# Kernel optimization log

Measured on AMD Instinct MI355X. Metric: run time of the kernel, lower is better.

The kernel has to match this reference:

```python
import jax, jax.numpy as jnp
import numpy as np

N, D_IN, D_OUT, E = 50000, 64, 64, 800000
NEG_SLOPE = 0.2  # PyG GATConv default leaky-relu slope


def setup_inputs() -> dict:
    key = jax.random.key(0)
    ks = jax.random.split(key, 11)
    s_in = 1.0 / np.sqrt(D_IN)
    s_out = 1.0 / np.sqrt(D_OUT)
    return {
        "x": jax.random.normal(ks[0], (N, D_IN), jnp.float32),
        "edge_index": jax.random.randint(ks[1], (2, E), 0, N, jnp.int32),
        "h": jax.random.normal(ks[2], (N, D_OUT), jnp.float32) * 0.1,
        "c": jax.random.normal(ks[3], (N, D_OUT), jnp.float32) * 0.1,
        "W": jax.random.normal(ks[4], (4, D_IN, D_OUT), jnp.float32) * s_in,
        "b": jax.random.normal(ks[5], (4, 1, D_OUT), jnp.float32) * 0.01,
        "Wsrc": jax.random.normal(ks[6], (4, D_OUT, D_OUT), jnp.float32) * s_out,
        "Wdst": jax.random.normal(ks[7], (4, D_OUT, D_OUT), jnp.float32) * s_out,
        "att_src": jax.random.normal(ks[8], (4, D_OUT), jnp.float32) * 0.1,
        "att_dst": jax.random.normal(ks[9], (4, D_OUT), jnp.float32) * 0.1,
        "gat_b": jax.random.normal(ks[10], (4, D_OUT), jnp.float32) * 0.01,
    }


def _gat(h, src, dst, Ws, Wd, a_s, a_d, bg, n):
    """GATConv(heads=1, add_self_loops=False) on edges src->dst."""
    hs = h @ Ws                      # [N, D] source-side projection
    hd = h @ Wd                      # [N, D] dest-side projection
    alpha_s = hs @ a_s               # [N]
    alpha_d = hd @ a_d               # [N]
    e = jax.nn.leaky_relu(alpha_s[src] + alpha_d[dst], NEG_SLOPE)  # [E]
    # numerically stable segment softmax over incoming edges per dst node
    m = jax.ops.segment_max(e, dst, num_segments=n)
    ex = jnp.exp(e - m[dst])
    denom = jax.ops.segment_sum(ex, dst, num_segments=n)
    w = ex / denom[dst]              # [E] attention weights
    out = jax.ops.segment_sum(w[:, None] * hs[src], dst, num_segments=n)
    return out + bg


def reference(x, edge_index, h, c, W, b, Wsrc, Wdst, att_src, att_dst, gat_b):
    src, dst = edge_index[0], edge_index[1]
    n = x.shape[0]

    def gate(g, act):
        pre = x @ W[g] + _gat(h, src, dst, Wsrc[g], Wdst[g],
                              att_src[g], att_dst[g], gat_b[g], n) + b[g]
        return act(pre)

    i = gate(0, jax.nn.sigmoid)
    f = gate(1, jax.nn.sigmoid)
    t = gate(2, jnp.tanh)
    c_new = f * c + i * t
    o = gate(3, jax.nn.sigmoid)   # output gate conv uses the OLD hidden state h
    h_new = o * jnp.tanh(c_new)
    return (h_new, c_new)
```

## Files before the change

kernel.cpp:

```cpp
#include <hip/hip_runtime.h>
#include <math.h>

#define NEG_SLOPE 0.2f

typedef float  f32x4 __attribute__((ext_vector_type(4)));
typedef short  s16x8 __attribute__((ext_vector_type(8)));

__device__ __forceinline__ unsigned short bfr(float a){
  unsigned u = __float_as_uint(a);
  return (unsigned short)((u + 0x7FFFu + ((u>>16)&1u)) >> 16);
}
__device__ __forceinline__ float bf2f(unsigned short s){
  return __uint_as_float(((unsigned)s)<<16);
}
__device__ __forceinline__ ushort4 packf4(float4 v){
  ushort4 r; r.x=bfr(v.x); r.y=bfr(v.y); r.z=bfr(v.z); r.w=bfr(v.w); return r;
}

__global__ void k_wvec_pack(const float* __restrict__ Wsrc, const float* __restrict__ Wdst,
                            const float* __restrict__ Wmain,
                            const float* __restrict__ att_src, const float* __restrict__ att_dst,
                            float* __restrict__ wvec,
                            unsigned short* __restrict__ pw, unsigned short* __restrict__ ps){
  int tid = threadIdx.x;
  if (blockIdx.x == 0){
    int v = tid >> 6, t = tid & 63;
    const float* M = (v<4) ? (Wsrc + v*4096) : (Wdst + (v-4)*4096);
    const float* a = (v<4) ? (att_src + v*64) : (att_dst + (v-4)*64);
    float s = 0.f;
    for (int k=0;k<64;++k) s += M[t*64+k]*a[k];
    wvec[v*64+t] = s;
  } else {
    int vv = (blockIdx.x-1)*512 + tid;
    if (vv < 2048){
      int l = vv & 63, u = vv >> 6;
      int ct = u & 3, ks = (u>>2)&1, g = u>>3;
      int col = ct*16 + (l&15);
      int r0  = ks*32 + (l>>4)*8;
      #pragma unroll
      for (int j=0;j<8;++j){
        pw[vv*8+j] = bfr(Wmain[g*4096 + (r0+j)*64 + col]);
        ps[vv*8+j] = bfr(Wsrc [g*4096 + (r0+j)*64 + col]);
      }
    }
  }
}

__global__ __launch_bounds__(256) void k_pack(
    const float* __restrict__ x, const float* __restrict__ h,
    const float* __restrict__ wvec,
    unsigned short* __restrict__ xb, unsigned short* __restrict__ hb,
    float* __restrict__ alphas, int N){
  __shared__ float hl[32*65];
  __shared__ float wl[8*65];
  int tid = threadIdx.x;
  int nbase = blockIdx.x*32;
  int nlim = min(32, N-nbase);
  int cnt = nlim*16;
  {
    const float4* hsrc = (const float4*)(h + (size_t)nbase*64);
    const float4* xsrc = (const float4*)(x + (size_t)nbase*64);
    ushort4* hdst = (ushort4*)(hb + (size_t)nbase*64);
    ushort4* xdst = (ushort4*)(xb + (size_t)nbase*64);
    for (int i=tid; i<cnt; i+=256){
      float4 v = hsrc[i];
      int n = i>>4, t4 = (i&15)*4;
      float* d = hl + n*65 + t4;
      d[0]=v.x; d[1]=v.y; d[2]=v.z; d[3]=v.w;
      hdst[i] = packf4(v);
      xdst[i] = packf4(xsrc[i]);
    }
    for (int i=tid; i<512; i+=256) wl[(i>>6)*65 + (i&63)] = wvec[i];
  }
  __syncthreads();
  int v = tid & 7, n = tid >> 3;
  if (n < nlim){
    const float* hp = hl + n*65;
    const float* wp = wl + v*65;
    float s = 0.f;
    #pragma unroll
    for (int t=0;t<64;++t) s += hp[t]*wp[t];
    alphas[(size_t)(nbase+n)*8 + v] = s;
  }
}

__global__ __launch_bounds__(256) void k_bcount(
    const int* __restrict__ ei, int* __restrict__ bcnt, int shift, int E){
  __shared__ int c[128];
  int tid = threadIdx.x;
  for (int i=tid;i<128;i+=256) c[i]=0;
  __syncthreads();
  int Q = E >> 2;
  const int4* d4 = (const int4*)(ei + E);
  long gs = (long)gridDim.x*256;
  for (long q=(long)blockIdx.x*256+tid; q<Q; q+=gs){
    int4 d = d4[q];
    atomicAdd(&c[d.x>>shift],1); atomicAdd(&c[d.y>>shift],1);
    atomicAdd(&c[d.z>>shift],1); atomicAdd(&c[d.w>>shift],1);
  }
  int tail = E - (Q<<2);
  if (blockIdx.x==0 && tid<tail) atomicAdd(&c[ei[E+(Q<<2)+tid]>>shift],1);
  __syncthreads();
  for (int i=tid;i<128;i+=256) if (c[i]) atomicAdd(&bcnt[i], c[i]);
}

__global__ void k_bscan(const int* __restrict__ bcnt, int* __restrict__ bbase,
                        int* __restrict__ bfill, int* __restrict__ rowptr,
                        int nbuck, int N, int E){
  __shared__ int s[128];
  int tid = threadIdx.x;
  int x = (tid<nbuck) ? bcnt[tid] : 0;
  s[tid] = x;
  __syncthreads();
  for (int off=1; off<128; off<<=1){
    int t = (tid>=off) ? s[tid-off] : 0;
    __syncthreads();
    s[tid] += t;
    __syncthreads();
  }
  if (tid<nbuck){ int e = s[tid]-x; bbase[tid]=e; bfill[tid]=e; }
  if (tid==0){ bbase[nbuck]=E; rowptr[N]=E; }
}

__global__ __launch_bounds__(256) void k_bin(
    const int* __restrict__ ei, int* __restrict__ bfill,
    int2* __restrict__ binned, int shift, int E){
  __shared__ int2 buf[2048];
  __shared__ int cnt[128], off[128], gbase[128];
  int tid = threadIdx.x;
  int c0 = blockIdx.x*2048;
  int m = min(2048, E - c0);
  if (m <= 0) return;
  for (int i=tid; i<128; i+=256) cnt[i] = 0;
  __syncthreads();
  int myb[8], myslot[8], mysrc[8], mydst[8];
  #pragma unroll
  for (int j=0;j<8;++j){
    int k = tid + j*256;
    if (k < m){
      int e = c0 + k;
      mysrc[j] = ei[e];
      mydst[j] = ei[E+e];
      int bkt = mydst[j] >> shift;
      myb[j] = bkt;
      myslot[j] = atomicAdd(&cnt[bkt], 1);
    } else myb[j] = -1;
  }
  __syncthreads();
  if (tid == 0){
    int acc = 0;
    for (int i=0;i<128;++i){ off[i] = acc; acc += cnt[i]; }
  }
  __syncthreads();
  #pragma unroll
  for (int j=0;j<8;++j)
    if (myb[j] >= 0) buf[off[myb[j]] + myslot[j]] = make_int2(mysrc[j], mydst[j]);
  if (tid < 128 && cnt[tid] > 0) gbase[tid] = atomicAdd(&bfill[tid], cnt[tid]);
  __syncthreads();
  for (int i=tid; i<m; i+=256){
    int2 p = buf[i];
    int bkt = p.y >> shift;
    binned[gbase[bkt] + (i - off[bkt])] = p;
  }
}

__global__ __launch_bounds__(1024) void k_place(
    const int2* __restrict__ binned, const int* __restrict__ bbase,
    int* __restrict__ rowptr, int* __restrict__ csr_src, int shift, int N){
  __shared__ int cnt[1024];
  __shared__ int tsum[1024];
  int tid = threadIdx.x;
  int d0 = blockIdx.x << shift;
  if (d0 >= N) return;
  int dpb = 1 << shift;
  int dlim = min(dpb, N - d0);
  if (tid < dpb) cnt[tid] = 0;
  __syncthreads();
  int base = bbase[blockIdx.x], end = bbase[blockIdx.x+1];
  for (int i = base + tid; i < end; i += 1024)
    atomicAdd(&cnt[binned[i].y - d0], 1);
  __syncthreads();
  int xv = (tid < dpb) ? cnt[tid] : 0;
  tsum[tid] = xv;
  __syncthreads();
  for (int off=1; off<1024; off<<=1){
    int t = (tid>=off) ? tsum[tid-off] : 0;
    __syncthreads();
    tsum[tid] += t;
    __syncthreads();
  }
  if (tid < dpb) cnt[tid] = tsum[tid] - xv + base;
  __syncthreads();
  if (tid < dlim) rowptr[d0+tid] = cnt[tid];
  __syncthreads();
  for (int i = base + tid; i < end; i += 1024){
    int2 p = binned[i];
    int pos = atomicAdd(&cnt[p.y - d0], 1);
    csr_src[pos] = p.x;
  }
}

__global__ __launch_bounds__(256) void k_agg(
    const int* __restrict__ csr_src, const int* __restrict__ rowptr,
    const float* __restrict__ alphas,
    const unsigned short* __restrict__ hb, unsigned short* __restrict__ aggb, int N){
  __shared__ float4 wb4[4][64];
  __shared__ int    sb[4][64];
  int wave = threadIdx.x>>6, lane = threadIdx.x&63;
  int dst = blockIdx.x*4 + wave;
  if (dst >= N) return;
  int base = rowptr[dst];
  int d = rowptr[dst+1] - base;
  float4 ad = ((const float4*)alphas)[dst*2+1];
  float ss0=0.f,ss1=0.f,ss2=0.f,ss3=0.f;
  float a0=0.f,a1=0.f,a2=0.f,a3=0.f;
  for (int c0=0; c0<d; c0+=64){
    int cnt = min(64, d-c0);
    if (lane < cnt){
      int s = csr_src[base+c0+lane];
      float4 as = ((const float4*)alphas)[(size_t)s*2];
      float e0=as.x+ad.x; e0 = e0>0.f ? e0 : NEG_SLOPE*e0; float x0=__expf(e0); ss0+=x0;
      float e1=as.y+ad.y; e1 = e1>0.f ? e1 : NEG_SLOPE*e1; float x1=__expf(e1); ss1+=x1;
      float e2=as.z+ad.z; e2 = e2>0.f ? e2 : NEG_SLOPE*e2; float x2=__expf(e2); ss2+=x2;
      float e3=as.w+ad.w; e3 = e3>0.f ? e3 : NEG_SLOPE*e3; float x3=__expf(e3); ss3+=x3;
      sb[wave][lane] = s;
      wb4[wave][lane] = make_float4(x0,x1,x2,x3);
    }
    asm volatile("" ::: "memory");
    int j = 0;
    for (; j+3 < cnt; j += 4){
      int s0_ = sb[wave][j],   s1_ = sb[wave][j+1];
      int s2_ = sb[wave][j+2], s3_ = sb[wave][j+3];
      float4 w0_ = wb4[wave][j],   w1_ = wb4[wave][j+1];
      float4 w2_ = wb4[wave][j+2], w3_ = wb4[wave][j+3];
      float h0_ = bf2f(hb[(size_t)s0_*64 + lane]);
      float h1_ = bf2f(hb[(size_t)s1_*64 + lane]);
      float h2_ = bf2f(hb[(size_t)s2_*64 + lane]);
      float h3_ = bf2f(hb[(size_t)s3_*64 + lane]);
      a0 += w0_.x*h0_; a1 += w0_.y*h0_; a2 += w0_.z*h0_; a3 += w0_.w*h0_;
      a0 += w1_.x*h1_; a1 += w1_.y*h1_; a2 += w1_.z*h1_; a3 += w1_.w*h1_;
      a0 += w2_.x*h2_; a1 += w2_.y*h2_; a2 += w2_.z*h2_; a3 += w2_.w*h2_;
      a0 += w3_.x*h3_; a1 += w3_.y*h3_; a2 += w3_.z*h3_; a3 += w3_.w*h3_;
    }
    for (; j < cnt; ++j){
      int s = sb[wave][j];
      float4 w = wb4[wave][j];
      float hv = bf2f(hb[(size_t)s*64 + lane]);
      a0 += w.x*hv; a1 += w.y*hv; a2 += w.z*hv; a3 += w.w*hv;
    }
    asm volatile("" ::: "memory");
  }
  #pragma unroll
  for (int off=32; off; off>>=1){
    ss0 += __shfl_xor(ss0, off, 64);
    ss1 += __shfl_xor(ss1, off, 64);
    ss2 += __shfl_xor(ss2, off, 64);
    ss3 += __shfl_xor(ss3, off, 64);
  }
  size_t o = (size_t)dst*64 + lane;
  size_t NE = (size_t)N*64;
  if (d>0){
    aggb[o]      = bfr(a0/ss0);
    aggb[NE+o]   = bfr(a1/ss1);
    aggb[2*NE+o] = bfr(a2/ss2);
    aggb[3*NE+o] = bfr(a3/ss3);
  } else {
    aggb[o] = 0; aggb[NE+o] = 0; aggb[2*NE+o] = 0; aggb[3*NE+o] = 0;
  }
}

__global__ __launch_bounds__(256) void k_fused(
    const unsigned short* __restrict__ xb, const unsigned short* __restrict__ aggb,
    const unsigned short* __restrict__ pw, const unsigned short* __restrict__ ps,
    const float* __restrict__ b, const float* __restrict__ gat_b,
    const float* __restrict__ c, float* __restrict__ out, int N){
  __shared__ float Pl[4][32][68];
  int tid = threadIdx.x, g = tid>>6, l = tid&63;
  int lr = l & 15;
  int lq = l >> 4;
  int nbase = blockIdx.x*32;
  int nlim = min(32, N-nbase);

  s16x8 BW[2][4], BS[2][4];
  #pragma unroll
  for (int ks=0; ks<2; ++ks){
    #pragma unroll
    for (int ct=0; ct<4; ++ct){
      size_t idx = ((size_t)((g*2+ks)*4+ct)*64 + l)*8;
      BW[ks][ct] = *(const s16x8*)(pw + idx);
      BS[ks][ct] = *(const s16x8*)(ps + idx);
    }
  }

  s16x8 AX[2][2], AG[2][2];
  #pragma unroll
  for (int rt=0; rt<2; ++rt){
    int row = nbase + rt*16 + lr;
    if (row >= N) row = N-1;
    #pragma unroll
    for (int ks=0; ks<2; ++ks){
      AX[rt][ks] = *(const s16x8*)(xb   + (size_t)row*64 + ks*32 + lq*8);
      AG[rt][ks] = *(const s16x8*)(aggb + ((size_t)g*N + row)*64 + ks*32 + lq*8);
    }
  }

  #pragma unroll
  for (int rt=0; rt<2; ++rt){
    #pragma unroll
    for (int ct=0; ct<4; ++ct){
      int col = ct*16 + lr;
      float bias = b[g*64 + col] + gat_b[g*64 + col];
      f32x4 acc = {bias, bias, bias, bias};
      #pragma unroll
      for (int ks=0; ks<2; ++ks){
        acc = __builtin_amdgcn_mfma_f32_16x16x32_bf16(AX[rt][ks], BW[ks][ct], acc, 0,0,0);
        acc = __builtin_amdgcn_mfma_f32_16x16x32_bf16(AG[rt][ks], BS[ks][ct], acc, 0,0,0);
      }
      #pragma unroll
      for (int r=0;r<4;++r)
        Pl[g][rt*16 + lq*4 + r][col] = acc[r];
    }
  }
  __syncthreads();

  size_t NE = (size_t)N*64;
  #pragma unroll
  for (int n=0; n<8; ++n){
    int node = g*8 + n;
    if (node < nlim){
      size_t o = (size_t)(nbase + node)*64 + l;
      float p0 = Pl[0][node][l];
      float p1 = Pl[1][node][l];
      float p2 = Pl[2][node][l];
      float p3 = Pl[3][node][l];
      float ig = 1.f/(1.f + __expf(-p0));
      float fg = 1.f/(1.f + __expf(-p1));
      float tg = tanhf(p2);
      float og = 1.f/(1.f + __expf(-p3));
      float cn = fg*c[o] + ig*tg;
      out[o]      = og*tanhf(cn);
      out[NE + o] = cn;
    }
  }
}

extern "C" void kernel_launch(void* const* d_in, const int* in_sizes, int n_in,
                              void* d_out, int out_size, void* d_ws, size_t ws_size,
                              hipStream_t stream){
  const float* x       = (const float*)d_in[0];
  const int*   ei      = (const int*)d_in[1];
  const float* h       = (const float*)d_in[2];
  const float* c       = (const float*)d_in[3];
  const float* W       = (const float*)d_in[4];
  const float* b       = (const float*)d_in[5];
  const float* Wsrc    = (const float*)d_in[6];
  const float* Wdst    = (const float*)d_in[7];
  const float* att_src = (const float*)d_in[8];
  const float* att_dst = (const float*)d_in[9];
  const float* gat_b   = (const float*)d_in[10];
  float* out = (float*)d_out;

  int N = in_sizes[0] / 64;
  int E = in_sizes[1] / 2;

  int shift = 9;
  while (((N + (1<<shift) - 1) >> shift) > 128) shift++;
  int nbuck = (N + (1<<shift) - 1) >> shift;

  unsigned short* aggb = (unsigned short*)d_ws;
  unsigned short* xb   = aggb + (size_t)4*N*64;
  unsigned short* hb   = xb   + (size_t)N*64;
  unsigned short* pw   = hb   + (size_t)N*64;
  unsigned short* ps   = pw   + 16384;
  float* alphas = (float*)(ps + 16384);
  int* csr_src  = (int*)(alphas + (size_t)N*8);
  int2* binned  = (int2*)(csr_src + ((E+3)&~3));
  int* rowptr   = (int*)(binned + E);
  int* bcnt     = rowptr + N + 1;
  int* bbase    = bcnt + 128;
  int* bfill    = bbase + 129;
  float* wvec   = (float*)(bfill + 128);

  hipMemsetAsync(bcnt, 0, 128*sizeof(int), stream);
  k_wvec_pack<<<9, 512, 0, stream>>>(Wsrc, Wdst, W, att_src, att_dst, wvec, pw, ps);
  k_pack  <<<(N+31)/32, 256, 0, stream>>>(x, h, wvec, xb, hb, alphas, N);
  k_bcount<<<256, 256, 0, stream>>>(ei, bcnt, shift, E);
  k_bscan <<<1, 128, 0, stream>>>(bcnt, bbase, bfill, rowptr, nbuck, N, E);
  k_bin   <<<(E + 2047)/2048, 256, 0, stream>>>(ei, bfill, binned, shift, E);
  k_place <<<nbuck, 1024, 0, stream>>>(binned, bbase, rowptr, csr_src, shift, N);
  k_agg   <<<(N+3)/4, 256, 0, stream>>>(csr_src, rowptr, alphas, hb, aggb, N);
  k_fused <<<(N+31)/32, 256, 0, stream>>>(xb, aggb, pw, ps, b, gat_b, c, out, N);
}
```

Before: 127.4 us.

## Fuse bucket counting into pack kernel and process two destinations per wave

The memset is replaced by zeroing the bucket counters inside k_wvec_pack, and the separate k_bcount kernel is merged into k_pack, which now also histograms the destination indices. This removes two launches from the chain. k_agg now has each wave handle two destination nodes at once, which raises memory-level parallelism on the gathers but does extra work when the two degrees differ. Each wave also uses more registers.

```diff
diff --git a/kernel.cpp b/kernel.cpp
--- a/kernel.cpp
+++ b/kernel.cpp
@@ -20,10 +20,11 @@
 __global__ void k_wvec_pack(const float* __restrict__ Wsrc, const float* __restrict__ Wdst,
                             const float* __restrict__ Wmain,
                             const float* __restrict__ att_src, const float* __restrict__ att_dst,
-                            float* __restrict__ wvec,
+                            float* __restrict__ wvec, int* __restrict__ bcnt,
                             unsigned short* __restrict__ pw, unsigned short* __restrict__ ps){
   int tid = threadIdx.x;
   if (blockIdx.x == 0){
+    if (tid < 128) bcnt[tid] = 0;
     int v = tid >> 6, t = tid & 63;
     const float* M = (v<4) ? (Wsrc + v*4096) : (Wdst + (v-4)*4096);
     const float* a = (v<4) ? (att_src + v*64) : (att_dst + (v-4)*64);
@@ -48,15 +49,17 @@
 
 __global__ __launch_bounds__(256) void k_pack(
     const float* __restrict__ x, const float* __restrict__ h,
-    const float* __restrict__ wvec,
+    const float* __restrict__ wvec, const int* __restrict__ ei,
     unsigned short* __restrict__ xb, unsigned short* __restrict__ hb,
-    float* __restrict__ alphas, int N){
+    float* __restrict__ alphas, int* __restrict__ bcnt, int shift, int N, int E){
   __shared__ float hl[32*65];
   __shared__ float wl[8*65];
+  __shared__ int   cb[128];
   int tid = threadIdx.x;
   int nbase = blockIdx.x*32;
   int nlim = min(32, N-nbase);
   int cnt = nlim*16;
+  if (tid < 128) cb[tid] = 0;
   {
     const float4* hsrc = (const float4*)(h + (size_t)nbase*64);
     const float4* xsrc = (const float4*)(x + (size_t)nbase*64);
@@ -82,26 +85,18 @@
     for (int t=0;t<64;++t) s += hp[t]*wp[t];
     alphas[(size_t)(nbase+n)*8 + v] = s;
   }
-}
-
-__global__ __launch_bounds__(256) void k_bcount(
-    const int* __restrict__ ei, int* __restrict__ bcnt, int shift, int E){
-  __shared__ int c[128];
-  int tid = threadIdx.x;
-  for (int i=tid;i<128;i+=256) c[i]=0;
-  __syncthreads();
   int Q = E >> 2;
   const int4* d4 = (const int4*)(ei + E);
   long gs = (long)gridDim.x*256;
   for (long q=(long)blockIdx.x*256+tid; q<Q; q+=gs){
     int4 d = d4[q];
-    atomicAdd(&c[d.x>>shift],1); atomicAdd(&c[d.y>>shift],1);
-    atomicAdd(&c[d.z>>shift],1); atomicAdd(&c[d.w>>shift],1);
+    atomicAdd(&cb[d.x>>shift],1); atomicAdd(&cb[d.y>>shift],1);
+    atomicAdd(&cb[d.z>>shift],1); atomicAdd(&cb[d.w>>shift],1);
   }
   int tail = E - (Q<<2);
-  if (blockIdx.x==0 && tid<tail) atomicAdd(&c[ei[E+(Q<<2)+tid]>>shift],1);
-  __syncthreads();
-  for (int i=tid;i<128;i+=256) if (c[i]) atomicAdd(&bcnt[i], c[i]);
+  if (blockIdx.x == 0 && tid < tail) atomicAdd(&cb[ei[E+(Q<<2)+tid]>>shift],1);
+  __syncthreads();
+  if (tid < 128 && cb[tid]) atomicAdd(&bcnt[tid], cb[tid]);
 }
 
 __global__ void k_bscan(const int* __restrict__ bcnt, int* __restrict__ bbase,
@@ -204,68 +199,109 @@
     const int* __restrict__ csr_src, const int* __restrict__ rowptr,
     const float* __restrict__ alphas,
     const unsigned short* __restrict__ hb, unsigned short* __restrict__ aggb, int N){
-  __shared__ float4 wb4[4][64];
-  __shared__ int    sb[4][64];
+  __shared__ float4 wb4[4][2][64];
+  __shared__ int    sb[4][2][64];
   int wave = threadIdx.x>>6, lane = threadIdx.x&63;
-  int dst = blockIdx.x*4 + wave;
-  if (dst >= N) return;
-  int base = rowptr[dst];
-  int d = rowptr[dst+1] - base;
-  float4 ad = ((const float4*)alphas)[dst*2+1];
-  float ss0=0.f,ss1=0.f,ss2=0.f,ss3=0.f;
-  float a0=0.f,a1=0.f,a2=0.f,a3=0.f;
-  for (int c0=0; c0<d; c0+=64){
-    int cnt = min(64, d-c0);
-    if (lane < cnt){
-      int s = csr_src[base+c0+lane];
-      float4 as = ((const float4*)alphas)[(size_t)s*2];
-      float e0=as.x+ad.x; e0 = e0>0.f ? e0 : NEG_SLOPE*e0; float x0=__expf(e0); ss0+=x0;
-      float e1=as.y+ad.y; e1 = e1>0.f ? e1 : NEG_SLOPE*e1; float x1=__expf(e1); ss1+=x1;
-      float e2=as.z+ad.z; e2 = e2>0.f ? e2 : NEG_SLOPE*e2; float x2=__expf(e2); ss2+=x2;
-      float e3=as.w+ad.w; e3 = e3>0.f ? e3 : NEG_SLOPE*e3; float x3=__expf(e3); ss3+=x3;
-      sb[wave][lane] = s;
-      wb4[wave][lane] = make_float4(x0,x1,x2,x3);
+  int dst0 = blockIdx.x*8 + wave*2;
+  if (dst0 >= N) return;
+  int dst1 = dst0 + 1;
+  bool has1 = dst1 < N;
+  int base0 = rowptr[dst0];
+  int d0 = rowptr[dst0+1] - base0;
+  int base1 = has1 ? rowptr[dst1] : 0;
+  int d1 = has1 ? rowptr[dst1+1] - base1 : 0;
+  float4 ad0 = ((const float4*)alphas)[(size_t)dst0*2+1];
+  float4 ad1 = has1 ? ((const float4*)alphas)[(size_t)dst1*2+1] : make_float4(0,0,0,0);
+  float p00=0.f,p01=0.f,p02=0.f,p03=0.f, q00=0.f,q01=0.f,q02=0.f,q03=0.f;
+  float a00=0.f,a01=0.f,a02=0.f,a03=0.f, b00=0.f,b01=0.f,b02=0.f,b03=0.f;
+  int dmax = max(d0, d1);
+  for (int c0=0; c0<dmax; c0+=64){
+    {
+      int rem = d0 - c0;
+      int s = 0; float4 w = make_float4(0,0,0,0);
+      if (lane < rem){
+        s = csr_src[base0+c0+lane];
+        float4 as = ((const float4*)alphas)[(size_t)s*2];
+        float e0=as.x+ad0.x; e0 = e0>0.f ? e0 : NEG_SLOPE*e0; w.x=__expf(e0);
+        float e1=as.y+ad0.y; e1 = e1>0.f ? e1 : NEG_SLOPE*e1; w.y=__expf(e1);
+        float e2=as.z+ad0.z; e2 = e2>0.f ? e2 : NEG_SLOPE*e2; w.z=__expf(e2);
+        float e3=as.w+ad0.w; e3 = e3>0.f ? e3 : NEG_SLOPE*e3; w.w=__expf(e3);
+      }
+      p00+=w.x; p01+=w.y; p02+=w.z; p03+=w.w;
+      sb[wave][0][lane] = s;
+      wb4[wave][0][lane] = w;
+    }
+    {
+      int rem = d1 - c0;
+      int s = 0; float4 w = make_float4(0,0,0,0);
+      if (lane < rem){
+        s = csr_src[base1+c0+lane];
+        float4 as = ((const float4*)alphas)[(size_t)s*2];
+        float e0=as.x+ad1.x; e0 = e0>0.f ? e0 : NEG_SLOPE*e0; w.x=__expf(e0);
+        float e1=as.y+ad1.y; e1 = e1>0.f ? e1 : NEG_SLOPE*e1; w.y=__expf(e1);
+        float e2=as.z+ad1.z; e2 = e2>0.f ? e2 : NEG_SLOPE*e2; w.z=__expf(e2);
+        float e3=as.w+ad1.w; e3 = e3>0.f ? e3 : NEG_SLOPE*e3; w.w=__expf(e3);
+      }
+      q00+=w.x; q01+=w.y; q02+=w.z; q03+=w.w;
+      sb[wave][1][lane] = s;
+      wb4[wave][1][lane] = w;
     }
     asm volatile("" ::: "memory");
+    int cc = min(64, dmax - c0);
     int j = 0;
-    for (; j+3 < cnt; j += 4){
-      int s0_ = sb[wave][j],   s1_ = sb[wave][j+1];
-      int s2_ = sb[wave][j+2], s3_ = sb[wave][j+3];
-      float4 w0_ = wb4[wave][j],   w1_ = wb4[wave][j+1];
-      float4 w2_ = wb4[wave][j+2], w3_ = wb4[wave][j+3];
-      float h0_ = bf2f(hb[(size_t)s0_*64 + lane]);
-      float h1_ = bf2f(hb[(size_t)s1_*64 + lane]);
-      float h2_ = bf2f(hb[(size_t)s2_*64 + lane]);
-      float h3_ = bf2f(hb[(size_t)s3_*64 + lane]);
-      a0 += w0_.x*h0_; a1 += w0_.y*h0_; a2 += w0_.z*h0_; a3 += w0_.w*h0_;
-      a0 += w1_.x*h1_; a1 += w1_.y*h1_; a2 += w1_.z*h1_; a3 += w1_.w*h1_;
-      a0 += w2_.x*h2_; a1 += w2_.y*h2_; a2 += w2_.z*h2_; a3 += w2_.w*h2_;
-      a0 += w3_.x*h3_; a1 += w3_.y*h3_; a2 += w3_.z*h3_; a3 += w3_.w*h3_;
-    }
-    for (; j < cnt; ++j){
-      int s = sb[wave][j];
-      float4 w = wb4[wave][j];
-      float hv = bf2f(hb[(size_t)s*64 + lane]);
-      a0 += w.x*hv; a1 += w.y*hv; a2 += w.z*hv; a3 += w.w*hv;
+    for (; j+1 < cc; j += 2){
+      int   sa0 = sb[wave][0][j],  sa1 = sb[wave][0][j+1];
+      int   sc0 = sb[wave][1][j],  sc1 = sb[wave][1][j+1];
+      float4 wa0 = wb4[wave][0][j], wa1 = wb4[wave][0][j+1];
+      float4 wc0 = wb4[wave][1][j], wc1 = wb4[wave][1][j+1];
+      float ha0 = bf2f(hb[(size_t)sa0*64 + lane]);
+      float ha1 = bf2f(hb[(size_t)sa1*64 + lane]);
+      float hc0 = bf2f(hb[(size_t)sc0*64 + lane]);
+      float hc1 = bf2f(hb[(size_t)sc1*64 + lane]);
+      a00 += wa0.x*ha0; a01 += wa0.y*ha0; a02 += wa0.z*ha0; a03 += wa0.w*ha0;
+      a00 += wa1.x*ha1; a01 += wa1.y*ha1; a02 += wa1.z*ha1; a03 += wa1.w*ha1;
+      b00 += wc0.x*hc0; b01 += wc0.y*hc0; b02 += wc0.z*hc0; b03 += wc0.w*hc0;
+      b00 += wc1.x*hc1; b01 += wc1.y*hc1; b02 += wc1.z*hc1; b03 += wc1.w*hc1;
+    }
+    for (; j < cc; ++j){
+      int   sa = sb[wave][0][j],  sc = sb[wave][1][j];
+      float4 wa = wb4[wave][0][j], wc = wb4[wave][1][j];
+      float ha = bf2f(hb[(size_t)sa*64 + lane]);
+      float hc = bf2f(hb[(size_t)sc*64 + lane]);
+      a00 += wa.x*ha; a01 += wa.y*ha; a02 += wa.z*ha; a03 += wa.w*ha;
+      b00 += wc.x*hc; b01 += wc.y*hc; b02 += wc.z*hc; b03 += wc.w*hc;
     }
     asm volatile("" ::: "memory");
   }
   #pragma unroll
   for (int off=32; off; off>>=1){
-    ss0 += __shfl_xor(ss0, off, 64);
-    ss1 += __shfl_xor(ss1, off, 64);
-    ss2 += __shfl_xor(ss2, off, 64);
-    ss3 += __shfl_xor(ss3, off, 64);
-  }
-  size_t o = (size_t)dst*64 + lane;
+    p00 += __shfl_xor(p00, off, 64); p01 += __shfl_xor(p01, off, 64);
+    p02 += __shfl_xor(p02, off, 64); p03 += __shfl_xor(p03, off, 64);
+    q00 += __shfl_xor(q00, off, 64); q01 += __shfl_xor(q01, off, 64);
+    q02 += __shfl_xor(q02, off, 64); q03 += __shfl_xor(q03, off, 64);
+  }
   size_t NE = (size_t)N*64;
-  if (d>0){
-    aggb[o]      = bfr(a0/ss0);
-    aggb[NE+o]   = bfr(a1/ss1);
-    aggb[2*NE+o] = bfr(a2/ss2);
-    aggb[3*NE+o] = bfr(a3/ss3);
-  } else {
-    aggb[o] = 0; aggb[NE+o] = 0; aggb[2*NE+o] = 0; aggb[3*NE+o] = 0;
+  {
+    size_t o = (size_t)dst0*64 + lane;
+    if (d0>0){
+      aggb[o]      = bfr(a00/p00);
+      aggb[NE+o]   = bfr(a01/p01);
+      aggb[2*NE+o] = bfr(a02/p02);
+      aggb[3*NE+o] = bfr(a03/p03);
+    } else {
+      aggb[o]=0; aggb[NE+o]=0; aggb[2*NE+o]=0; aggb[3*NE+o]=0;
+    }
+  }
+  if (has1){
+    size_t o = (size_t)dst1*64 + lane;
+    if (d1>0){
+      aggb[o]      = bfr(b00/q00);
+      aggb[NE+o]   = bfr(b01/q01);
+      aggb[2*NE+o] = bfr(b02/q02);
+      aggb[3*NE+o] = bfr(b03/q03);
+    } else {
+      aggb[o]=0; aggb[NE+o]=0; aggb[2*NE+o]=0; aggb[3*NE+o]=0;
+    }
   }
 }
 
@@ -381,13 +417,11 @@
   int* bfill    = bbase + 129;
   float* wvec   = (float*)(bfill + 128);
 
-  hipMemsetAsync(bcnt, 0, 128*sizeof(int), stream);
-  k_wvec_pack<<<9, 512, 0, stream>>>(Wsrc, Wdst, W, att_src, att_dst, wvec, pw, ps);
-  k_pack  <<<(N+31)/32, 256, 0, stream>>>(x, h, wvec, xb, hb, alphas, N);
-  k_bcount<<<256, 256, 0, stream>>>(ei, bcnt, shift, E);
+  k_wvec_pack<<<9, 512, 0, stream>>>(Wsrc, Wdst, W, att_src, att_dst, wvec, bcnt, pw, ps);
+  k_pack  <<<(N+31)/32, 256, 0, stream>>>(x, h, wvec, ei, xb, hb, alphas, bcnt, shift, N, E);
   k_bscan <<<1, 128, 0, stream>>>(bcnt, bbase, bfill, rowptr, nbuck, N, E);
   k_bin   <<<(E + 2047)/2048, 256, 0, stream>>>(ei, bfill, binned, shift, E);
   k_place <<<nbuck, 1024, 0, stream>>>(binned, bbase, rowptr, csr_src, shift, N);
-  k_agg   <<<(N+3)/4, 256, 0, stream>>>(csr_src, rowptr, alphas, hb, aggb, N);
+  k_agg   <<<(N+7)/8, 256, 0, stream>>>(csr_src, rowptr, alphas, hb, aggb, N);
   k_fused <<<(N+31)/32, 256, 0, stream>>>(xb, aggb, pw, ps, b, gat_b, c, out, N);
 }
```

Measured after the change: 133.9 us. 5.2% more time.

## Precompute edge attention weights in placement kernel and fuse bucket count into pack

Applied to the files above, without the earlier changes.

Edge attention exponentials are now computed in the CSR placement kernel, which already visits every edge, and stored as fp16 per-edge weights. The aggregation kernel no longer does the random gather of source alphas or the exp math. The bucket-count kernel is folded into the pack kernel, and the memset is replaced by zeroing inside the weight-pack kernel, which cuts two launches. The trade-off is an extra E×8-byte weight write and read, plus fp16 rounding of the unnormalized exp weights, which could overflow if logits are large.

```diff
diff --git a/kernel.cpp b/kernel.cpp
--- a/kernel.cpp
+++ b/kernel.cpp
@@ -5,6 +5,8 @@
 
 typedef float  f32x4 __attribute__((ext_vector_type(4)));
 typedef short  s16x8 __attribute__((ext_vector_type(8)));
+
+union H4 { ushort4 u; _Float16 h[4]; };
 
 __device__ __forceinline__ unsigned short bfr(float a){
   unsigned u = __float_as_uint(a);
@@ -20,10 +22,11 @@
 __global__ void k_wvec_pack(const float* __restrict__ Wsrc, const float* __restrict__ Wdst,
                             const float* __restrict__ Wmain,
                             const float* __restrict__ att_src, const float* __restrict__ att_dst,
-                            float* __restrict__ wvec,
+                            float* __restrict__ wvec, int* __restrict__ bcnt,
                             unsigned short* __restrict__ pw, unsigned short* __restrict__ ps){
   int tid = threadIdx.x;
   if (blockIdx.x == 0){
+    if (tid < 128) bcnt[tid] = 0;
     int v = tid >> 6, t = tid & 63;
     const float* M = (v<4) ? (Wsrc + v*4096) : (Wdst + (v-4)*4096);
     const float* a = (v<4) ? (att_src + v*64) : (att_dst + (v-4)*64);
@@ -48,15 +51,17 @@
 
 __global__ __launch_bounds__(256) void k_pack(
     const float* __restrict__ x, const float* __restrict__ h,
-    const float* __restrict__ wvec,
+    const float* __restrict__ wvec, const int* __restrict__ ei,
     unsigned short* __restrict__ xb, unsigned short* __restrict__ hb,
-    float* __restrict__ alphas, int N){
+    float* __restrict__ alphas, int* __restrict__ bcnt, int shift, int N, int E){
   __shared__ float hl[32*65];
   __shared__ float wl[8*65];
+  __shared__ int   cb[128];
   int tid = threadIdx.x;
   int nbase = blockIdx.x*32;
   int nlim = min(32, N-nbase);
   int cnt = nlim*16;
+  if (tid < 128) cb[tid] = 0;
   {
     const float4* hsrc = (const float4*)(h + (size_t)nbase*64);
     const float4* xsrc = (const float4*)(x + (size_t)nbase*64);
@@ -82,26 +87,18 @@
     for (int t=0;t<64;++t) s += hp[t]*wp[t];
     alphas[(size_t)(nbase+n)*8 + v] = s;
   }
-}
-
-__global__ __launch_bounds__(256) void k_bcount(
-    const int* __restrict__ ei, int* __restrict__ bcnt, int shift, int E){
-  __shared__ int c[128];
-  int tid = threadIdx.x;
-  for (int i=tid;i<128;i+=256) c[i]=0;
-  __syncthreads();
   int Q = E >> 2;
   const int4* d4 = (const int4*)(ei + E);
   long gs = (long)gridDim.x*256;
   for (long q=(long)blockIdx.x*256+tid; q<Q; q+=gs){
     int4 d = d4[q];
-    atomicAdd(&c[d.x>>shift],1); atomicAdd(&c[d.y>>shift],1);
-    atomicAdd(&c[d.z>>shift],1); atomicAdd(&c[d.w>>shift],1);
+    atomicAdd(&cb[d.x>>shift],1); atomicAdd(&cb[d.y>>shift],1);
+    atomicAdd(&cb[d.z>>shift],1); atomicAdd(&cb[d.w>>shift],1);
   }
   int tail = E - (Q<<2);
-  if (blockIdx.x==0 && tid<tail) atomicAdd(&c[ei[E+(Q<<2)+tid]>>shift],1);
-  __syncthreads();
-  for (int i=tid;i<128;i+=256) if (c[i]) atomicAdd(&bcnt[i], c[i]);
+  if (blockIdx.x == 0 && tid < tail) atomicAdd(&cb[ei[E+(Q<<2)+tid]>>shift],1);
+  __syncthreads();
+  if (tid < 128 && cb[tid]) atomicAdd(&bcnt[tid], cb[tid]);
 }
 
 __global__ void k_bscan(const int* __restrict__ bcnt, int* __restrict__ bbase,
@@ -166,15 +163,19 @@
 
 __global__ __launch_bounds__(1024) void k_place(
     const int2* __restrict__ binned, const int* __restrict__ bbase,
-    int* __restrict__ rowptr, int* __restrict__ csr_src, int shift, int N){
+    const float* __restrict__ alphas,
+    int* __restrict__ rowptr, int* __restrict__ csr_src,
+    ushort4* __restrict__ csr_w, int shift, int N){
   __shared__ int cnt[1024];
   __shared__ int tsum[1024];
+  __shared__ float4 adl[1024];
   int tid = threadIdx.x;
   int d0 = blockIdx.x << shift;
   if (d0 >= N) return;
   int dpb = 1 << shift;
   int dlim = min(dpb, N - d0);
   if (tid < dpb) cnt[tid] = 0;
+  if (tid < dlim) adl[tid] = ((const float4*)alphas)[(size_t)(d0+tid)*2 + 1];
   __syncthreads();
   int base = bbase[blockIdx.x], end = bbase[blockIdx.x+1];
   for (int i = base + tid; i < end; i += 1024)
@@ -195,14 +196,27 @@
   __syncthreads();
   for (int i = base + tid; i < end; i += 1024){
     int2 p = binned[i];
-    int pos = atomicAdd(&cnt[p.y - d0], 1);
+    int loc = p.y - d0;
+    int pos = atomicAdd(&cnt[loc], 1);
+    float4 as = ((const float4*)alphas)[(size_t)p.x*2];
+    float4 ad = adl[loc];
+    float e0=as.x+ad.x; e0 = e0>0.f ? e0 : NEG_SLOPE*e0;
+    float e1=as.y+ad.y; e1 = e1>0.f ? e1 : NEG_SLOPE*e1;
+    float e2=as.z+ad.z; e2 = e2>0.f ? e2 : NEG_SLOPE*e2;
+    float e3=as.w+ad.w; e3 = e3>0.f ? e3 : NEG_SLOPE*e3;
+    H4 t;
+    t.h[0] = (_Float16)__expf(e0);
+    t.h[1] = (_Float16)__expf(e1);
+    t.h[2] = (_Float16)__expf(e2);
+    t.h[3] = (_Float16)__expf(e3);
     csr_src[pos] = p.x;
+    csr_w[pos] = t.u;
   }
 }
 
 __global__ __launch_bounds__(256) void k_agg(
-    const int* __restrict__ csr_src, const int* __restrict__ rowptr,
-    const float* __restrict__ alphas,
+    const int* __restrict__ csr_src, const ushort4* __restrict__ csr_w,
+    const int* __restrict__ rowptr,
     const unsigned short* __restrict__ hb, unsigned short* __restrict__ aggb, int N){
   __shared__ float4 wb4[4][64];
   __shared__ int    sb[4][64];
@@ -211,21 +225,19 @@
   if (dst >= N) return;
   int base = rowptr[dst];
   int d = rowptr[dst+1] - base;
-  float4 ad = ((const float4*)alphas)[dst*2+1];
   float ss0=0.f,ss1=0.f,ss2=0.f,ss3=0.f;
   float a0=0.f,a1=0.f,a2=0.f,a3=0.f;
   for (int c0=0; c0<d; c0+=64){
     int cnt = min(64, d-c0);
+    int s = 0; float4 w = make_float4(0,0,0,0);
     if (lane < cnt){
-      int s = csr_src[base+c0+lane];
-      float4 as = ((const float4*)alphas)[(size_t)s*2];
-      float e0=as.x+ad.x; e0 = e0>0.f ? e0 : NEG_SLOPE*e0; float x0=__expf(e0); ss0+=x0;
-      float e1=as.y+ad.y; e1 = e1>0.f ? e1 : NEG_SLOPE*e1; float x1=__expf(e1); ss1+=x1;
-      float e2=as.z+ad.z; e2 = e2>0.f ? e2 : NEG_SLOPE*e2; float x2=__expf(e2); ss2+=x2;
-      float e3=as.w+ad.w; e3 = e3>0.f ? e3 : NEG_SLOPE*e3; float x3=__expf(e3); ss3+=x3;
-      sb[wave][lane] = s;
-      wb4[wave][lane] = make_float4(x0,x1,x2,x3);
-    }
+      s = csr_src[base+c0+lane];
+      H4 t; t.u = csr_w[base+c0+lane];
+      w = make_float4((float)t.h[0], (float)t.h[1], (float)t.h[2], (float)t.h[3]);
+    }
+    ss0 += w.x; ss1 += w.y; ss2 += w.z; ss3 += w.w;
+    sb[wave][lane] = s;
+    wb4[wave][lane] = w;
     asm volatile("" ::: "memory");
     int j = 0;
     for (; j+3 < cnt; j += 4){
@@ -243,10 +255,10 @@
       a0 += w3_.x*h3_; a1 += w3_.y*h3_; a2 += w3_.z*h3_; a3 += w3_.w*h3_;
     }
     for (; j < cnt; ++j){
-      int s = sb[wave][j];
-      float4 w = wb4[wave][j];
-      float hv = bf2f(hb[(size_t)s*64 + lane]);
-      a0 += w.x*hv; a1 += w.y*hv; a2 += w.z*hv; a3 += w.w*hv;
+      int sj = sb[wave][j];
+      float4 wj = wb4[wave][j];
+      float hv = bf2f(hb[(size_t)sj*64 + lane]);
+      a0 += wj.x*hv; a1 += wj.y*hv; a2 += wj.z*hv; a3 += wj.w*hv;
     }
     asm volatile("" ::: "memory");
   }
@@ -375,19 +387,18 @@
   float* alphas = (float*)(ps + 16384);
   int* csr_src  = (int*)(alphas + (size_t)N*8);
   int2* binned  = (int2*)(csr_src + ((E+3)&~3));
-  int* rowptr   = (int*)(binned + E);
+  ushort4* csr_w= (ushort4*)(binned + E);
+  int* rowptr   = (int*)(csr_w + E);
   int* bcnt     = rowptr + N + 1;
   int* bbase    = bcnt + 128;
   int* bfill    = bbase + 129;
   float* wvec   = (float*)(bfill + 128);
 
-  hipMemsetAsync(bcnt, 0, 128*sizeof(int), stream);
-  k_wvec_pack<<<9, 512, 0, stream>>>(Wsrc, Wdst, W, att_src, att_dst, wvec, pw, ps);
-  k_pack  <<<(N+31)/32, 256, 0, stream>>>(x, h, wvec, xb, hb, alphas, N);
-  k_bcount<<<256, 256, 0, stream>>>(ei, bcnt, shift, E);
+  k_wvec_pack<<<9, 512, 0, stream>>>(Wsrc, Wdst, W, att_src, att_dst, wvec, bcnt, pw, ps);
+  k_pack  <<<(N+31)/32, 256, 0, stream>>>(x, h, wvec, ei, xb, hb, alphas, bcnt, shift, N, E);
   k_bscan <<<1, 128, 0, stream>>>(bcnt, bbase, bfill, rowptr, nbuck, N, E);
   k_bin   <<<(E + 2047)/2048, 256, 0, stream>>>(ei, bfill, binned, shift, E);
-  k_place <<<nbuck, 1024, 0, stream>>>(binned, bbase, rowptr, csr_src, shift, N);
-  k_agg   <<<(N+3)/4, 256, 0, stream>>>(csr_src, rowptr, alphas, hb, aggb, N);
+  k_place <<<nbuck, 1024, 0, stream>>>(binned, bbase, alphas, rowptr, csr_src, csr_w, shift, N);
+  k_agg   <<<(N+3)/4, 256, 0, stream>>>(csr_src, csr_w, rowptr, hb, aggb, N);
   k_fused <<<(N+31)/32, 256, 0, stream>>>(xb, aggb, pw, ps, b, gat_b, c, out, N);
 }
```

After: 144.4 us. 1.13x slower.

## Fuse bucket counting into pack kernel, drop memset, unroll aggregation by eight

Applied to the files above, without the earlier changes.

The destination-bucket histogram is folded into k_pack, so each of its many blocks counts a grid-strided slice of edges into shared memory before flushing to global. The bcnt zeroing moves into k_wvec_pack, which removes the memset and the separate k_bcount launch. The aggregation inner loop gains an 8-way unrolled gather stage so more independent hb loads are in flight per wave. Costs: roughly 1563 blocks each issue up to 128 global atomics at the end instead of 256 blocks, and the wider unroll raises register pressure in k_agg.

```diff
diff --git a/kernel.cpp b/kernel.cpp
--- a/kernel.cpp
+++ b/kernel.cpp
@@ -20,10 +20,11 @@
 __global__ void k_wvec_pack(const float* __restrict__ Wsrc, const float* __restrict__ Wdst,
                             const float* __restrict__ Wmain,
                             const float* __restrict__ att_src, const float* __restrict__ att_dst,
-                            float* __restrict__ wvec,
+                            float* __restrict__ wvec, int* __restrict__ bcnt,
                             unsigned short* __restrict__ pw, unsigned short* __restrict__ ps){
   int tid = threadIdx.x;
   if (blockIdx.x == 0){
+    if (tid < 128) bcnt[tid] = 0;
     int v = tid >> 6, t = tid & 63;
     const float* M = (v<4) ? (Wsrc + v*4096) : (Wdst + (v-4)*4096);
     const float* a = (v<4) ? (att_src + v*64) : (att_dst + (v-4)*64);
@@ -48,15 +49,17 @@
 
 __global__ __launch_bounds__(256) void k_pack(
     const float* __restrict__ x, const float* __restrict__ h,
-    const float* __restrict__ wvec,
+    const float* __restrict__ wvec, const int* __restrict__ ei,
     unsigned short* __restrict__ xb, unsigned short* __restrict__ hb,
-    float* __restrict__ alphas, int N){
+    float* __restrict__ alphas, int* __restrict__ bcnt, int shift, int N, int E){
   __shared__ float hl[32*65];
   __shared__ float wl[8*65];
+  __shared__ int   cb[128];
   int tid = threadIdx.x;
   int nbase = blockIdx.x*32;
   int nlim = min(32, N-nbase);
   int cnt = nlim*16;
+  if (tid < 128) cb[tid] = 0;
   {
     const float4* hsrc = (const float4*)(h + (size_t)nbase*64);
     const float4* xsrc = (const float4*)(x + (size_t)nbase*64);
@@ -82,26 +85,18 @@
     for (int t=0;t<64;++t) s += hp[t]*wp[t];
     alphas[(size_t)(nbase+n)*8 + v] = s;
   }
-}
-
-__global__ __launch_bounds__(256) void k_bcount(
-    const int* __restrict__ ei, int* __restrict__ bcnt, int shift, int E){
-  __shared__ int c[128];
-  int tid = threadIdx.x;
-  for (int i=tid;i<128;i+=256) c[i]=0;
-  __syncthreads();
   int Q = E >> 2;
   const int4* d4 = (const int4*)(ei + E);
   long gs = (long)gridDim.x*256;
   for (long q=(long)blockIdx.x*256+tid; q<Q; q+=gs){
     int4 d = d4[q];
-    atomicAdd(&c[d.x>>shift],1); atomicAdd(&c[d.y>>shift],1);
-    atomicAdd(&c[d.z>>shift],1); atomicAdd(&c[d.w>>shift],1);
+    atomicAdd(&cb[d.x>>shift],1); atomicAdd(&cb[d.y>>shift],1);
+    atomicAdd(&cb[d.z>>shift],1); atomicAdd(&cb[d.w>>shift],1);
   }
   int tail = E - (Q<<2);
-  if (blockIdx.x==0 && tid<tail) atomicAdd(&c[ei[E+(Q<<2)+tid]>>shift],1);
-  __syncthreads();
-  for (int i=tid;i<128;i+=256) if (c[i]) atomicAdd(&bcnt[i], c[i]);
+  if (blockIdx.x == 0 && tid < tail) atomicAdd(&cb[ei[E+(Q<<2)+tid]>>shift],1);
+  __syncthreads();
+  if (tid < 128 && cb[tid]) atomicAdd(&bcnt[tid], cb[tid]);
 }
 
 __global__ void k_bscan(const int* __restrict__ bcnt, int* __restrict__ bbase,
@@ -211,7 +206,7 @@
   if (dst >= N) return;
   int base = rowptr[dst];
   int d = rowptr[dst+1] - base;
-  float4 ad = ((const float4*)alphas)[dst*2+1];
+  float4 ad = ((const float4*)alphas)[(size_t)dst*2+1];
   float ss0=0.f,ss1=0.f,ss2=0.f,ss3=0.f;
   float a0=0.f,a1=0.f,a2=0.f,a3=0.f;
   for (int c0=0; c0<d; c0+=64){
@@ -228,25 +223,35 @@
     }
     asm volatile("" ::: "memory");
     int j = 0;
+    for (; j+7 < cnt; j += 8){
+      int   s_[8]; float4 w_[8]; float h_[8];
+      #pragma unroll
+      for (int u=0;u<8;++u){ s_[u] = sb[wave][j+u]; w_[u] = wb4[wave][j+u]; }
+      #pragma unroll
+      for (int u=0;u<8;++u) h_[u] = bf2f(hb[(size_t)s_[u]*64 + lane]);
+      #pragma unroll
+      for (int u=0;u<8;++u){
+        a0 += w_[u].x*h_[u]; a1 += w_[u].y*h_[u];
+        a2 += w_[u].z*h_[u]; a3 += w_[u].w*h_[u];
+      }
+    }
     for (; j+3 < cnt; j += 4){
-      int s0_ = sb[wave][j],   s1_ = sb[wave][j+1];
-      int s2_ = sb[wave][j+2], s3_ = sb[wave][j+3];
-      float4 w0_ = wb4[wave][j],   w1_ = wb4[wave][j+1];
-      float4 w2_ = wb4[wave][j+2], w3_ = wb4[wave][j+3];
-      float h0_ = bf2f(hb[(size_t)s0_*64 + lane]);
-      float h1_ = bf2f(hb[(size_t)s1_*64 + lane]);
-      float h2_ = bf2f(hb[(size_t)s2_*64 + lane]);
-      float h3_ = bf2f(hb[(size_t)s3_*64 + lane]);
-      a0 += w0_.x*h0_; a1 += w0_.y*h0_; a2 += w0_.z*h0_; a3 += w0_.w*h0_;
-      a0 += w1_.x*h1_; a1 += w1_.y*h1_; a2 += w1_.z*h1_; a3 += w1_.w*h1_;
-      a0 += w2_.x*h2_; a1 += w2_.y*h2_; a2 += w2_.z*h2_; a3 += w2_.w*h2_;
-      a0 += w3_.x*h3_; a1 += w3_.y*h3_; a2 += w3_.z*h3_; a3 += w3_.w*h3_;
+      int   s_[4]; float4 w_[4]; float h_[4];
+      #pragma unroll
+      for (int u=0;u<4;++u){ s_[u] = sb[wave][j+u]; w_[u] = wb4[wave][j+u]; }
+      #pragma unroll
+      for (int u=0;u<4;++u) h_[u] = bf2f(hb[(size_t)s_[u]*64 + lane]);
+      #pragma unroll
+      for (int u=0;u<4;++u){
+        a0 += w_[u].x*h_[u]; a1 += w_[u].y*h_[u];
+        a2 += w_[u].z*h_[u]; a3 += w_[u].w*h_[u];
+      }
     }
     for (; j < cnt; ++j){
-      int s = sb[wave][j];
-      float4 w = wb4[wave][j];
-      float hv = bf2f(hb[(size_t)s*64 + lane]);
-      a0 += w.x*hv; a1 += w.y*hv; a2 += w.z*hv; a3 += w.w*hv;
+      int sj = sb[wave][j];
+      float4 wj = wb4[wave][j];
+      float hv = bf2f(hb[(size_t)sj*64 + lane]);
+      a0 += wj.x*hv; a1 += wj.y*hv; a2 += wj.z*hv; a3 += wj.w*hv;
     }
     asm volatile("" ::: "memory");
   }
@@ -381,10 +386,8 @@
   int* bfill    = bbase + 129;
   float* wvec   = (float*)(bfill + 128);
 
-  hipMemsetAsync(bcnt, 0, 128*sizeof(int), stream);
-  k_wvec_pack<<<9, 512, 0, stream>>>(Wsrc, Wdst, W, att_src, att_dst, wvec, pw, ps);
-  k_pack  <<<(N+31)/32, 256, 0, stream>>>(x, h, wvec, xb, hb, alphas, N);
-  k_bcount<<<256, 256, 0, stream>>>(ei, bcnt, shift, E);
+  k_wvec_pack<<<9, 512, 0, stream>>>(Wsrc, Wdst, W, att_src, att_dst, wvec, bcnt, pw, ps);
+  k_pack  <<<(N+31)/32, 256, 0, stream>>>(x, h, wvec, ei, xb, hb, alphas, bcnt, shift, N, E);
   k_bscan <<<1, 128, 0, stream>>>(bcnt, bbase, bfill, rowptr, nbuck, N, E);
   k_bin   <<<(E + 2047)/2048, 256, 0, stream>>>(ei, bfill, binned, shift, E);
   k_place <<<nbuck, 1024, 0, stream>>>(binned, bbase, rowptr, csr_src, shift, N);
```

Result: slower. 130.0 us (+2.1%).
